# Kernel optimization log

Measured on AMD Instinct MI355X. Metric: run time of the kernel, lower is better.

## Reference

```python
import jax, jax.numpy as jnp
import numpy as np

N = 100000
E = 1600000
HID = 128
EPS = 1e-8


def _linear_params(key, fan_in, fan_out, bias=True, gain=1.0):
    kw, kb = jax.random.split(key)
    bound = gain / np.sqrt(fan_in)
    W = jax.random.uniform(kw, (fan_in, fan_out), jnp.float32, -bound, bound)
    if bias:
        b = jax.random.uniform(kb, (fan_out,), jnp.float32, -bound, bound)
        return W, b
    return W


def setup_inputs() -> dict:
    key = jax.random.key(0)
    ks = jax.random.split(key, 12)
    h = jax.random.normal(ks[0], (N, HID), jnp.float32)
    coord = jax.random.normal(ks[1], (N, 3), jnp.float32)
    edge_index = jax.random.randint(ks[2], (2, E), 0, N, jnp.int64)
    # edge_mlp: Linear(2*HID+1 -> HID), SiLU, Linear(HID -> HID), SiLU
    We1, be1 = _linear_params(ks[3], 2 * HID + 1, HID)
    We2, be2 = _linear_params(ks[4], HID, HID)
    # node_mlp: Linear(2*HID -> HID), SiLU, Linear(HID -> HID)
    Wn1, bn1 = _linear_params(ks[5], 2 * HID, HID)
    Wn2, bn2 = _linear_params(ks[6], HID, HID)
    # coord_mlp: Linear(HID -> HID), SiLU, Linear(HID -> 1, no bias, xavier gain=0.001)
    Wc1, bc1 = _linear_params(ks[7], HID, HID)
    Wc2 = _linear_params(ks[8], HID, 1, bias=False, gain=0.001 * np.sqrt(6.0 * HID / (HID + 1)))
    return {
        "h": h, "edge_index": edge_index, "coord": coord,
        "We1": We1, "be1": be1, "We2": We2, "be2": be2,
        "Wn1": Wn1, "bn1": bn1, "Wn2": Wn2, "bn2": bn2,
        "Wc1": Wc1, "bc1": bc1, "Wc2": Wc2,
    }


def _egcl(h, edge_index, coord, We1, be1, We2, be2, Wn1, bn1, Wn2, bn2, Wc1, bc1, Wc2):
    row, col = edge_index[0], edge_index[1]
    n = h.shape[0]
    # coord2radial (normalize=True, detach on norm)
    coord_diff = coord[row] - coord[col]                       # [E,3]
    radial = jnp.sum(coord_diff ** 2, axis=1, keepdims=True)   # [E,1]
    norm = jax.lax.stop_gradient(jnp.sqrt(radial)) + EPS
    coord_diff = coord_diff / norm
    # edge_model (no edge_attr, no attention)
    edge_in = jnp.concatenate([h[row], h[col], radial], axis=1)  # [E, 2H+1]
    m = jax.nn.silu(edge_in @ We1 + be1)
    m = jax.nn.silu(m @ We2 + be2)                               # [E,H]
    # coord_model (coords_agg='mean', tanh=False)
    phi_x = jax.nn.silu(m @ Wc1 + bc1) @ Wc2                     # [E,1]
    trans = coord_diff * phi_x                                   # [E,3]
    agg_c = jax.ops.segment_sum(trans, row, num_segments=n)
    cnt = jax.ops.segment_sum(jnp.ones((trans.shape[0],), trans.dtype), row, num_segments=n)
    agg_c = agg_c / jnp.clip(cnt, 1.0, None)[:, None]
    coord_out = coord + agg_c
    # node_model (residual=True)
    agg_h = jax.ops.segment_sum(m, row, num_segments=n)          # [N,H]
    node_in = jnp.concatenate([h, agg_h], axis=1)
    out = jax.nn.silu(node_in @ Wn1 + bn1) @ Wn2 + bn2
    h_out = h + out
    return h_out, coord_out


def reference(h, edge_index, coord, We1, be1, We2, be2, Wn1, bn1, Wn2, bn2, Wc1, bc1, Wc2):
    return _egcl(h, edge_index, coord, We1, be1, We2, be2, Wn1, bn1, Wn2, bn2, Wc1, bc1, Wc2)
```

## Files before the change

### kernel.cpp

```cpp
#include <hip/hip_runtime.h>

#define NN 100000
#define NE 1600000
#define HD 128
#define EPSV 1e-8f
#define EB 64
#define LPAD 136
#define CPAD 264

typedef unsigned short ushort_t;
typedef __attribute__((ext_vector_type(8))) short bf16x8;
typedef __attribute__((ext_vector_type(4))) float f32x4;

__device__ __forceinline__ float silu_f(float x) {
    return x * __builtin_amdgcn_rcpf(1.0f + __expf(-x));
}
__device__ __forceinline__ float b2f(unsigned short u) {
    union { unsigned int i; float f; } v; v.i = ((unsigned int)u) << 16; return v.f;
}
__device__ __forceinline__ unsigned short f2b(float f) {
    union { float f; unsigned int i; } v; v.f = f;
    unsigned int r = v.i + 0x7fff + ((v.i >> 16) & 1);
    return (unsigned short)(r >> 16);
}
__device__ __forceinline__ unsigned int cvt_pk_bf16(float lo, float hi) {
    unsigned int r;
    asm("v_cvt_pk_bf16_f32 %0, %1, %2" : "=v"(r) : "v"(lo), "v"(hi));
    return r;
}

extern "C" __global__ __launch_bounds__(256)
void k_prep(const float* __restrict__ We2, const float* __restrict__ Wc1,
            const float* __restrict__ We1, const float* __restrict__ Wn1,
            const float* __restrict__ Wn2,
            ushort_t* __restrict__ We2T, ushort_t* __restrict__ Wc1T,
            ushort_t* __restrict__ WabT, ushort_t* __restrict__ Wn1T,
            ushort_t* __restrict__ Wn2T)
{
    int id = blockIdx.x * 256 + threadIdx.x;
    if (id < 16384) {
        int n = id >> 7, k = id & 127;
        We2T[id] = f2b(We2[k * HD + n]);
    } else if (id < 32768) {
        int r = id - 16384; int n = r >> 7, k = r & 127;
        Wc1T[r] = f2b(Wc1[k * HD + n]);
    } else if (id < 65536) {
        int r = id - 32768; int j = r >> 7, k = r & 127;
        float v = (j < 128) ? We1[k * HD + j] : We1[(size_t)(128 + k) * HD + (j - 128)];
        WabT[r] = f2b(v);
    } else if (id < 98304) {
        int r = id - 65536; int j = r >> 8, k = r & 255;
        Wn1T[r] = f2b(Wn1[(size_t)k * HD + j]);
    } else if (id < 114688) {
        int r = id - 98304; int j = r >> 7, k = r & 127;
        Wn2T[r] = f2b(Wn2[k * HD + j]);
    }
}

extern "C" __global__ __launch_bounds__(256)
void k_hist(const int* __restrict__ ei, int* __restrict__ deg)
{
    int e = blockIdx.x * 256 + threadIdx.x;
    atomicAdd(&deg[ei[e]], 1);
}

extern "C" __global__ __launch_bounds__(1024)
void k_scan1(const int* __restrict__ deg, int* __restrict__ bsum)
{
    __shared__ int wsum[16];
    const int tid = threadIdx.x;
    const int lane = tid & 63, w = tid >> 6;
    int i = blockIdx.x * 1024 + tid;
    int v = (i < NN) ? deg[i] : 0;
#pragma unroll
    for (int off = 32; off > 0; off >>= 1) v += __shfl_xor(v, off, 64);
    if (lane == 0) wsum[w] = v;
    __syncthreads();
    if (tid == 0) {
        int s = 0;
#pragma unroll
        for (int k = 0; k < 16; k++) s += wsum[k];
        bsum[blockIdx.x] = s;
    }
}

extern "C" __global__ __launch_bounds__(128)
void k_scan2(const int* __restrict__ bsum, int* __restrict__ boff, int nb)
{
    __shared__ int wsum2[2];
    const int tid = threadIdx.x;
    const int lane = tid & 63, w = tid >> 6;
    int v = (tid < nb) ? bsum[tid] : 0;
    int s = v;
#pragma unroll
    for (int off = 1; off < 64; off <<= 1) {
        int t = __shfl_up(s, off, 64);
        if (lane >= off) s += t;
    }
    if (lane == 63) wsum2[w] = s;
    __syncthreads();
    int excl = ((w == 1) ? wsum2[0] : 0) + s - v;
    if (tid < nb) boff[tid] = excl;
}

extern "C" __global__ __launch_bounds__(1024)
void k_scan3(const int* __restrict__ deg, const int* __restrict__ boff,
             int* __restrict__ cursor)
{
    __shared__ int wsum[16];
    const int tid = threadIdx.x;
    const int lane = tid & 63, w = tid >> 6;
    int i = blockIdx.x * 1024 + tid;
    int v = (i < NN) ? deg[i] : 0;
    int s = v;
#pragma unroll
    for (int off = 1; off < 64; off <<= 1) {
        int t = __shfl_up(s, off, 64);
        if (lane >= off) s += t;
    }
    if (lane == 63) wsum[w] = s;
    __syncthreads();
    if (w == 0) {
        int ws = (lane < 16) ? wsum[lane] : 0;
#pragma unroll
        for (int off = 1; off < 16; off <<= 1) {
            int t = __shfl_up(ws, off, 64);
            if (lane >= off) ws += t;
        }
        if (lane < 16) wsum[lane] = ws;
    }
    __syncthreads();
    int excl = boff[blockIdx.x] + ((w > 0) ? wsum[w - 1] : 0) + s - v;
    if (i < NN) cursor[i] = excl;
}

extern "C" __global__ __launch_bounds__(256)
void k_sortids(const int* __restrict__ ei, int* __restrict__ cursor,
               int2* __restrict__ rc)
{
    int e = blockIdx.x * 256 + threadIdx.x;
    int r = ei[e], c = ei[NE + e];
    int slot = atomicAdd(&cursor[r], 1);
    rc[slot] = make_int2(r, c);
}

extern "C" __global__ __launch_bounds__(256)
void k_ab(const float* __restrict__ h, const ushort_t* __restrict__ WabT,
          const float* __restrict__ be1,
          ushort_t* __restrict__ A, ushort_t* __restrict__ B)
{
    __shared__ ushort_t hs[64][LPAD] __attribute__((aligned(16)));
    const int tid = threadIdx.x;
    const int n0 = blockIdx.x * 64;
    {
        int r = tid >> 2, seg = tid & 3;
        int n = n0 + r; if (n >= NN) n = n0;
        const float4* src = (const float4*)(h + (size_t)n * HD + seg * 32);
        uint2* dst = (uint2*)&hs[r][seg * 32];
#pragma unroll
        for (int i = 0; i < 8; i++) {
            float4 v = src[i];
            uint2 p; p.x = cvt_pk_bf16(v.x, v.y); p.y = cvt_pk_bf16(v.z, v.w);
            dst[i] = p;
        }
    }
    __syncthreads();
    const int wave = tid >> 6, lane = tid & 63;
    const int lr = lane & 15, lg = lane >> 4;
    f32x4 acc[16];
#pragma unroll
    for (int nt = 0; nt < 16; nt++) acc[nt] = (f32x4){0.f, 0.f, 0.f, 0.f};
#pragma unroll
    for (int ks = 0; ks < 4; ks++) {
        bf16x8 hf8 = *(const bf16x8*)&hs[wave * 16 + lr][ks * 32 + lg * 8];
#pragma unroll
        for (int nt = 0; nt < 16; nt++) {
            bf16x8 wf = *(const bf16x8*)(WabT + (size_t)(nt * 16 + lr) * HD + ks * 32 + lg * 8);
            acc[nt] = __builtin_amdgcn_mfma_f32_16x16x32_bf16(wf, hf8, acc[nt], 0, 0, 0);
        }
    }
    const int node = n0 + wave * 16 + lr;
    if (node < NN) {
#pragma unroll
        for (int nt = 0; nt < 16; nt++) {
            float4 bias = (nt < 8) ? ((const float4*)be1)[nt * 4 + lg]
                                   : (float4){0.f, 0.f, 0.f, 0.f};
            uint2 pk;
            pk.x = cvt_pk_bf16(acc[nt][0] + bias.x, acc[nt][1] + bias.y);
            pk.y = cvt_pk_bf16(acc[nt][2] + bias.z, acc[nt][3] + bias.w);
            if (nt < 8)
                *(uint2*)(A + (size_t)node * HD + nt * 16 + lg * 4) = pk;
            else
                *(uint2*)(B + (size_t)node * HD + (nt - 8) * 16 + lg * 4) = pk;
        }
    }
}

extern "C" __global__ __launch_bounds__(128, 4)
void k_edge(const int2* __restrict__ rc, const float* __restrict__ coord,
            const ushort_t* __restrict__ A, const ushort_t* __restrict__ B,
            const float* __restrict__ WeL, const float* __restrict__ be2,
            const ushort_t* __restrict__ We2T,
            const ushort_t* __restrict__ Wc1T,
            const float* __restrict__ bc1, const float* __restrict__ Wc2,
            float* __restrict__ agg_h, float* __restrict__ agg_c)
{
    __shared__ ushort_t m_lds[EB][LPAD] __attribute__((aligned(16)));
    __shared__ float cd_lds[EB][3];
    __shared__ int rows_s[EB];
    __shared__ float bias_lds[384] __attribute__((aligned(16)));
    __shared__ float wel_lds[128] __attribute__((aligned(16)));

    const int tid = threadIdx.x;
    const int e  = tid >> 1;
    const int hf = tid & 1;
    const int wave = tid >> 6, lane = tid & 63;
    const int lr = lane & 15, lg = lane >> 4;

    {
        int i = tid;
        bias_lds[i]       = (i < 128) ? be2[i] : 0.f;
        bias_lds[128 + i] = bc1[i];
        if (i < 128) bias_lds[256 + i] = Wc2[i];
        wel_lds[i] = WeL[i];
    }
    int2 rce = rc[blockIdx.x * EB + e];
    const int row = rce.x, col = rce.y;

    float c0 = coord[(size_t)row * 3 + 0] - coord[(size_t)col * 3 + 0];
    float c1 = coord[(size_t)row * 3 + 1] - coord[(size_t)col * 3 + 1];
    float c2 = coord[(size_t)row * 3 + 2] - coord[(size_t)col * 3 + 2];
    float radial = c0 * c0 + c1 * c1 + c2 * c2;
    if (hf == 0) {
        rows_s[e] = row;
        float inv = __builtin_amdgcn_rcpf(sqrtf(radial) + EPSV);
        cd_lds[e][0] = c0 * inv; cd_lds[e][1] = c1 * inv; cd_lds[e][2] = c2 * inv;
    }
    __syncthreads();

    {
        const bf16x8* A8 = (const bf16x8*)(A + (size_t)row * HD + hf * 64);
        const bf16x8* B8 = (const bf16x8*)(B + (size_t)col * HD + hf * 64);
        const float4* WL4 = (const float4*)wel_lds + hf * 16;
#pragma unroll
        for (int i = 0; i < 8; i++) {
            bf16x8 av = A8[i], bv = B8[i];
            float4 w0 = WL4[2 * i], w1 = WL4[2 * i + 1];
            float v0 = silu_f(b2f((ushort_t)av[0]) + b2f((ushort_t)bv[0]) + radial * w0.x);
            float v1 = silu_f(b2f((ushort_t)av[1]) + b2f((ushort_t)bv[1]) + radial * w0.y);
            float v2 = silu_f(b2f((ushort_t)av[2]) + b2f((ushort_t)bv[2]) + radial * w0.z);
            float v3 = silu_f(b2f((ushort_t)av[3]) + b2f((ushort_t)bv[3]) + radial * w0.w);
            float v4 = silu_f(b2f((ushort_t)av[4]) + b2f((ushort_t)bv[4]) + radial * w1.x);
            float v5 = silu_f(b2f((ushort_t)av[5]) + b2f((ushort_t)bv[5]) + radial * w1.y);
            float v6 = silu_f(b2f((ushort_t)av[6]) + b2f((ushort_t)bv[6]) + radial * w1.z);
            float v7 = silu_f(b2f((ushort_t)av[7]) + b2f((ushort_t)bv[7]) + radial * w1.w);
            uint4 p;
            p.x = cvt_pk_bf16(v0, v1); p.y = cvt_pk_bf16(v2, v3);
            p.z = cvt_pk_bf16(v4, v5); p.w = cvt_pk_bf16(v6, v7);
            *(uint4*)&m_lds[e][hf * 64 + i * 8] = p;
        }
    }

    f32x4 acc[2][8];
#pragma unroll
    for (int mt = 0; mt < 2; mt++)
#pragma unroll
        for (int nt = 0; nt < 8; nt++) acc[mt][nt] = (f32x4){0.f, 0.f, 0.f, 0.f};
#pragma unroll
    for (int ks = 0; ks < 4; ks++) {
        bf16x8 mf0 = *(const bf16x8*)&m_lds[wave * 32 + lr][ks * 32 + lg * 8];
        bf16x8 mf1 = *(const bf16x8*)&m_lds[wave * 32 + 16 + lr][ks * 32 + lg * 8];
#pragma unroll
        for (int nt = 0; nt < 8; nt++) {
            bf16x8 wf = *(const bf16x8*)(We2T + (size_t)(nt * 16 + lr) * HD + ks * 32 + lg * 8);
            acc[0][nt] = __builtin_amdgcn_mfma_f32_16x16x32_bf16(wf, mf0, acc[0][nt], 0, 0, 0);
            acc[1][nt] = __builtin_amdgcn_mfma_f32_16x16x32_bf16(wf, mf1, acc[1][nt], 0, 0, 0);
        }
    }
#pragma unroll
    for (int nt = 0; nt < 8; nt++) {
        float4 be2v = *(const float4*)&bias_lds[nt * 16 + lg * 4];
#pragma unroll
        for (int mt = 0; mt < 2; mt++) {
            float v0 = silu_f(acc[mt][nt][0] + be2v.x);
            float v1 = silu_f(acc[mt][nt][1] + be2v.y);
            float v2 = silu_f(acc[mt][nt][2] + be2v.z);
            float v3 = silu_f(acc[mt][nt][3] + be2v.w);
            uint2 pk; pk.x = cvt_pk_bf16(v0, v1); pk.y = cvt_pk_bf16(v2, v3);
            *(uint2*)&m_lds[wave * 32 + mt * 16 + lr][nt * 16 + lg * 4] = pk;
        }
    }

#pragma unroll
    for (int mt = 0; mt < 2; mt++)
#pragma unroll
        for (int nt = 0; nt < 8; nt++) acc[mt][nt] = (f32x4){0.f, 0.f, 0.f, 0.f};
#pragma unroll
    for (int ks = 0; ks < 4; ks++) {
        bf16x8 mf0 = *(const bf16x8*)&m_lds[wave * 32 + lr][ks * 32 + lg * 8];
        bf16x8 mf1 = *(const bf16x8*)&m_lds[wave * 32 + 16 + lr][ks * 32 + lg * 8];
#pragma unroll
        for (int nt = 0; nt < 8; nt++) {
            bf16x8 wf = *(const bf16x8*)(Wc1T + (size_t)(nt * 16 + lr) * HD + ks * 32 + lg * 8);
            acc[0][nt] = __builtin_amdgcn_mfma_f32_16x16x32_bf16(wf, mf0, acc[0][nt], 0, 0, 0);
            acc[1][nt] = __builtin_amdgcn_mfma_f32_16x16x32_bf16(wf, mf1, acc[1][nt], 0, 0, 0);
        }
    }

    float ph0 = 0.f, ph1 = 0.f;
#pragma unroll
    for (int nt = 0; nt < 8; nt++) {
        float4 bc1v = *(const float4*)&bias_lds[128 + nt * 16 + lg * 4];
        float4 wc2v = *(const float4*)&bias_lds[256 + nt * 16 + lg * 4];
        ph0 += silu_f(acc[0][nt][0] + bc1v.x) * wc2v.x
             + silu_f(acc[0][nt][1] + bc1v.y) * wc2v.y
             + silu_f(acc[0][nt][2] + bc1v.z) * wc2v.z
             + silu_f(acc[0][nt][3] + bc1v.w) * wc2v.w;
        ph1 += silu_f(acc[1][nt][0] + bc1v.x) * wc2v.x
             + silu_f(acc[1][nt][1] + bc1v.y) * wc2v.y
             + silu_f(acc[1][nt][2] + bc1v.z) * wc2v.z
             + silu_f(acc[1][nt][3] + bc1v.w) * wc2v.w;
    }
    ph0 += __shfl_xor(ph0, 16, 64); ph0 += __shfl_xor(ph0, 32, 64);
    ph1 += __shfl_xor(ph1, 16, 64); ph1 += __shfl_xor(ph1, 32, 64);
    if (lg == 0) {
        int e0 = wave * 32 + lr, e1 = e0 + 16;
        cd_lds[e0][0] *= ph0; cd_lds[e0][1] *= ph0; cd_lds[e0][2] *= ph0;
        cd_lds[e1][0] *= ph1; cd_lds[e1][1] *= ph1; cd_lds[e1][2] *= ph1;
    }

    __syncthreads();

    {
        const int j = tid;
        float acc_r = 0.f;
        int cur = rows_s[0];
        for (int es = 0; es < EB; es++) {
            int r = rows_s[es];
            if (r != cur) {
                atomicAdd(&agg_h[(size_t)cur * HD + j], acc_r);
                acc_r = 0.f; cur = r;
            }
            acc_r += b2f(m_lds[es][j]);
        }
        atomicAdd(&agg_h[(size_t)cur * HD + j], acc_r);
    }
    if (wave == 0) {
        int c = lane >> 4, sub = lane & 15;
        if (c < 3) {
            const int es0 = sub * 4, es1 = es0 + 4;
            float acc_r = 0.f;
            int cur = rows_s[es0];
            for (int es = es0; es < es1; es++) {
                int r = rows_s[es];
                if (r != cur) {
                    atomicAdd(&agg_c[(size_t)cur * 3 + c], acc_r);
                    acc_r = 0.f; cur = r;
                }
                acc_r += cd_lds[es][c];
            }
            atomicAdd(&agg_c[(size_t)cur * 3 + c], acc_r);
        }
    }
}

extern "C" __global__ __launch_bounds__(256)
void k_node(const float* __restrict__ h, const ushort_t* __restrict__ Wn1T,
            const float* __restrict__ bn1, const ushort_t* __restrict__ Wn2T,
            const float* __restrict__ bn2, const float* __restrict__ coord,
            const int* __restrict__ deg,
            float* __restrict__ hout ,
            float* __restrict__ cout )
{
    __shared__ ushort_t cs[64][CPAD] __attribute__((aligned(16)));
    __shared__ ushort_t us[64][LPAD] __attribute__((aligned(16)));
    const int tid = threadIdx.x;
    const int n0 = blockIdx.x * 64;
    {
        int r = tid >> 2, seg = tid & 3;
        int n = n0 + r; if (n >= NN) n = n0;
        const float4* s0 = (const float4*)(h + (size_t)n * HD + seg * 32);
        const float4* s1 = (const float4*)(hout + (size_t)n * HD + seg * 32);
        uint2* d0 = (uint2*)&cs[r][seg * 32];
        uint2* d1 = (uint2*)&cs[r][128 + seg * 32];
#pragma unroll
        for (int i = 0; i < 8; i++) {
            float4 v = s0[i];
            uint2 p; p.x = cvt_pk_bf16(v.x, v.y); p.y = cvt_pk_bf16(v.z, v.w);
            d0[i] = p;
            float4 w = s1[i];
            uint2 q; q.x = cvt_pk_bf16(w.x, w.y); q.y = cvt_pk_bf16(w.z, w.w);
            d1[i] = q;
        }
    }
    __syncthreads();
    const int wave = tid >> 6, lane = tid & 63;
    const int lr = lane & 15, lg = lane >> 4;

    f32x4 acc[8];
#pragma unroll
    for (int nt = 0; nt < 8; nt++) acc[nt] = (f32x4){0.f, 0.f, 0.f, 0.f};
#pragma unroll
    for (int ks = 0; ks < 8; ks++) {
        bf16x8 cf = *(const bf16x8*)&cs[wave * 16 + lr][ks * 32 + lg * 8];
#pragma unroll
        for (int nt = 0; nt < 8; nt++) {
            bf16x8 wf = *(const bf16x8*)(Wn1T + (size_t)(nt * 16 + lr) * 256 + ks * 32 + lg * 8);
            acc[nt] = __builtin_amdgcn_mfma_f32_16x16x32_bf16(wf, cf, acc[nt], 0, 0, 0);
        }
    }
#pragma unroll
    for (int nt = 0; nt < 8; nt++) {
        float4 b1 = ((const float4*)bn1)[nt * 4 + lg];
        float v0 = silu_f(acc[nt][0] + b1.x);
        float v1 = silu_f(acc[nt][1] + b1.y);
        float v2 = silu_f(acc[nt][2] + b1.z);
        float v3 = silu_f(acc[nt][3] + b1.w);
        uint2 pk; pk.x = cvt_pk_bf16(v0, v1); pk.y = cvt_pk_bf16(v2, v3);
        *(uint2*)&us[wave * 16 + lr][nt * 16 + lg * 4] = pk;
    }

    f32x4 acc2[8];
#pragma unroll
    for (int nt = 0; nt < 8; nt++) acc2[nt] = (f32x4){0.f, 0.f, 0.f, 0.f};
#pragma unroll
    for (int ks = 0; ks < 4; ks++) {
        bf16x8 uf = *(const bf16x8*)&us[wave * 16 + lr][ks * 32 + lg * 8];
#pragma unroll
        for (int nt = 0; nt < 8; nt++) {
            bf16x8 wf = *(const bf16x8*)(Wn2T + (size_t)(nt * 16 + lr) * HD + ks * 32 + lg * 8);
            acc2[nt] = __builtin_amdgcn_mfma_f32_16x16x32_bf16(wf, uf, acc2[nt], 0, 0, 0);
        }
    }
    const int node = n0 + wave * 16 + lr;
    if (node < NN) {
#pragma unroll
        for (int nt = 0; nt < 8; nt++) {
            float4 b2 = ((const float4*)bn2)[nt * 4 + lg];
            size_t idx = (size_t)node * HD + nt * 16 + lg * 4;
            float4 hv = *(const float4*)(h + idx);
            float4 o;
            o.x = hv.x + acc2[nt][0] + b2.x;
            o.y = hv.y + acc2[nt][1] + b2.y;
            o.z = hv.z + acc2[nt][2] + b2.z;
            o.w = hv.w + acc2[nt][3] + b2.w;
            *(float4*)(hout + idx) = o;
        }
        if (lg == 0) {
            float invc = __builtin_amdgcn_rcpf(fmaxf((float)deg[node], 1.0f));
#pragma unroll
            for (int i = 0; i < 3; i++) {
                size_t idx = (size_t)node * 3 + i;
                cout[idx] = coord[idx] + cout[idx] * invc;
            }
        }
    }
}

extern "C" void kernel_launch(void* const* d_in, const int* in_sizes, int n_in,
                              void* d_out, int out_size, void* d_ws, size_t ws_size,
                              hipStream_t stream)
{
    const float* h     = (const float*)d_in[0];
    const int*   ei    = (const int*)d_in[1];
    const float* coord = (const float*)d_in[2];
    const float* We1   = (const float*)d_in[3];
    const float* be1   = (const float*)d_in[4];
    const float* We2   = (const float*)d_in[5];
    const float* be2   = (const float*)d_in[6];
    const float* Wn1   = (const float*)d_in[7];
    const float* bn1   = (const float*)d_in[8];
    const float* Wn2   = (const float*)d_in[9];
    const float* bn2   = (const float*)d_in[10];
    const float* Wc1   = (const float*)d_in[11];
    const float* bc1   = (const float*)d_in[12];
    const float* Wc2   = (const float*)d_in[13];

    float* out   = (float*)d_out;
    float* agg_h = out;
    float* agg_c = out + (size_t)NN * HD;

    ushort_t* A    = (ushort_t*)d_ws;
    ushort_t* B    = A + (size_t)NN * HD;
    ushort_t* We2T = B + (size_t)NN * HD;
    ushort_t* Wc1T = We2T + 16384;
    ushort_t* WabT = Wc1T + 16384;
    ushort_t* Wn1T = WabT + 32768;
    ushort_t* Wn2T = Wn1T + 32768;
    int* deg    = (int*)(Wn2T + 16384);
    int* cursor = deg + NN;
    int* bsum   = cursor + NN;
    int* boff   = bsum + 128;
    int2* rc    = (int2*)(boff + 128);
    const float* WeL = We1 + (size_t)2 * HD * HD;

    const int scan_nb = (NN + 1023) / 1024;

    hipMemsetAsync(d_out, 0, (size_t)out_size * sizeof(float), stream);
    hipMemsetAsync(deg, 0, (size_t)NN * sizeof(int), stream);

    k_prep<<<448, 256, 0, stream>>>(We2, Wc1, We1, Wn1, Wn2,
                                    We2T, Wc1T, WabT, Wn1T, Wn2T);
    k_hist<<<NE / 256, 256, 0, stream>>>(ei, deg);
    k_ab<<<(NN + 63) / 64, 256, 0, stream>>>(h, WabT, be1, A, B);
    k_scan1<<<scan_nb, 1024, 0, stream>>>(deg, bsum);
    k_scan2<<<1, 128, 0, stream>>>(bsum, boff, scan_nb);
    k_scan3<<<scan_nb, 1024, 0, stream>>>(deg, boff, cursor);
    k_sortids<<<NE / 256, 256, 0, stream>>>(ei, cursor, rc);
    k_edge<<<NE / EB, 128, 0, stream>>>(rc, coord, A, B, WeL, be2,
                                        We2T, Wc1T, bc1, Wc2, agg_h, agg_c);
    k_node<<<(NN + 63) / 64, 256, 0, stream>>>(h, Wn1T, bn1, Wn2T, bn2, coord,
                                               deg, agg_h, agg_c);
}
```

Before: 889.1 us.

## Fuse prep with histogram, drop scan2 launch, load MFMA fragments directly

Merges the weight-prep and degree-histogram kernels into one launch, and folds the block-offset scan into k_scan3 by having each block sum the preceding block sums itself. k_ab and k_node now build MFMA fragments directly from global fp32 memory instead of staging through LDS with a barrier. s_setprio is added around the MFMA loops in k_edge. The aim is fewer launches and less LDS traffic, at the cost of uncoalesced fragment loads from global memory and redundant bsum reads in the scan.

After: 897.9 us. No clear change (+1.0%).

```diff
diff --git a/kernel.cpp b/kernel.cpp
--- a/kernel.cpp
+++ b/kernel.cpp
@@ -6,7 +6,6 @@
 #define EPSV 1e-8f
 #define EB 64
 #define LPAD 136
-#define CPAD 264
 
 typedef unsigned short ushort_t;
 typedef __attribute__((ext_vector_type(8))) short bf16x8;
@@ -28,16 +27,26 @@
     asm("v_cvt_pk_bf16_f32 %0, %1, %2" : "=v"(r) : "v"(lo), "v"(hi));
     return r;
 }
+__device__ __forceinline__ bf16x8 frag_from_f32(const float* p) {
+    float4 a0 = *(const float4*)p;
+    float4 a1 = *(const float4*)(p + 4);
+    union { bf16x8 v; uint4 u; } r;
+    r.u.x = cvt_pk_bf16(a0.x, a0.y); r.u.y = cvt_pk_bf16(a0.z, a0.w);
+    r.u.z = cvt_pk_bf16(a1.x, a1.y); r.u.w = cvt_pk_bf16(a1.z, a1.w);
+    return r.v;
+}
 
 extern "C" __global__ __launch_bounds__(256)
-void k_prep(const float* __restrict__ We2, const float* __restrict__ Wc1,
-            const float* __restrict__ We1, const float* __restrict__ Wn1,
-            const float* __restrict__ Wn2,
-            ushort_t* __restrict__ We2T, ushort_t* __restrict__ Wc1T,
-            ushort_t* __restrict__ WabT, ushort_t* __restrict__ Wn1T,
-            ushort_t* __restrict__ Wn2T)
+void k_prep_hist(const int* __restrict__ ei, int* __restrict__ deg,
+                 const float* __restrict__ We2, const float* __restrict__ Wc1,
+                 const float* __restrict__ We1, const float* __restrict__ Wn1,
+                 const float* __restrict__ Wn2,
+                 ushort_t* __restrict__ We2T, ushort_t* __restrict__ Wc1T,
+                 ushort_t* __restrict__ WabT, ushort_t* __restrict__ Wn1T,
+                 ushort_t* __restrict__ Wn2T)
 {
     int id = blockIdx.x * 256 + threadIdx.x;
+    atomicAdd(&deg[ei[id]], 1);
     if (id < 16384) {
         int n = id >> 7, k = id & 127;
         We2T[id] = f2b(We2[k * HD + n]);
@@ -57,13 +66,6 @@
     }
 }
 
-extern "C" __global__ __launch_bounds__(256)
-void k_hist(const int* __restrict__ ei, int* __restrict__ deg)
-{
-    int e = blockIdx.x * 256 + threadIdx.x;
-    atomicAdd(&deg[ei[e]], 1);
-}
-
 extern "C" __global__ __launch_bounds__(1024)
 void k_scan1(const int* __restrict__ deg, int* __restrict__ bsum)
 {
@@ -84,30 +86,12 @@
     }
 }
 
-extern "C" __global__ __launch_bounds__(128)
-void k_scan2(const int* __restrict__ bsum, int* __restrict__ boff, int nb)
-{
-    __shared__ int wsum2[2];
-    const int tid = threadIdx.x;
-    const int lane = tid & 63, w = tid >> 6;
-    int v = (tid < nb) ? bsum[tid] : 0;
-    int s = v;
-#pragma unroll
-    for (int off = 1; off < 64; off <<= 1) {
-        int t = __shfl_up(s, off, 64);
-        if (lane >= off) s += t;
-    }
-    if (lane == 63) wsum2[w] = s;
-    __syncthreads();
-    int excl = ((w == 1) ? wsum2[0] : 0) + s - v;
-    if (tid < nb) boff[tid] = excl;
-}
-
 extern "C" __global__ __launch_bounds__(1024)
-void k_scan3(const int* __restrict__ deg, const int* __restrict__ boff,
+void k_scan3(const int* __restrict__ deg, const int* __restrict__ bsum,
              int* __restrict__ cursor)
 {
     __shared__ int wsum[16];
+    __shared__ int boff_s;
     const int tid = threadIdx.x;
     const int lane = tid & 63, w = tid >> 6;
     int i = blockIdx.x * 1024 + tid;
@@ -119,6 +103,13 @@
         if (lane >= off) s += t;
     }
     if (lane == 63) wsum[w] = s;
+    if (w == 0) {
+        int a = 0;
+        for (int k = lane; k < blockIdx.x; k += 64) a += bsum[k];
+#pragma unroll
+        for (int off = 32; off > 0; off >>= 1) a += __shfl_xor(a, off, 64);
+        if (lane == 0) boff_s = a;
+    }
     __syncthreads();
     if (w == 0) {
         int ws = (lane < 16) ? wsum[lane] : 0;
@@ -130,7 +121,7 @@
         if (lane < 16) wsum[lane] = ws;
     }
     __syncthreads();
-    int excl = boff[blockIdx.x] + ((w > 0) ? wsum[w - 1] : 0) + s - v;
+    int excl = boff_s + ((w > 0) ? wsum[w - 1] : 0) + s - v;
     if (i < NN) cursor[i] = excl;
 }
 
@@ -149,37 +140,25 @@
           const float* __restrict__ be1,
           ushort_t* __restrict__ A, ushort_t* __restrict__ B)
 {
-    __shared__ ushort_t hs[64][LPAD] __attribute__((aligned(16)));
     const int tid = threadIdx.x;
     const int n0 = blockIdx.x * 64;
-    {
-        int r = tid >> 2, seg = tid & 3;
-        int n = n0 + r; if (n >= NN) n = n0;
-        const float4* src = (const float4*)(h + (size_t)n * HD + seg * 32);
-        uint2* dst = (uint2*)&hs[r][seg * 32];
-#pragma unroll
-        for (int i = 0; i < 8; i++) {
-            float4 v = src[i];
-            uint2 p; p.x = cvt_pk_bf16(v.x, v.y); p.y = cvt_pk_bf16(v.z, v.w);
-            dst[i] = p;
-        }
-    }
-    __syncthreads();
     const int wave = tid >> 6, lane = tid & 63;
     const int lr = lane & 15, lg = lane >> 4;
+    const int node = n0 + wave * 16 + lr;
+    const int nsrc = (node < NN) ? node : (NN - 1);
+
     f32x4 acc[16];
 #pragma unroll
     for (int nt = 0; nt < 16; nt++) acc[nt] = (f32x4){0.f, 0.f, 0.f, 0.f};
 #pragma unroll
     for (int ks = 0; ks < 4; ks++) {
-        bf16x8 hf8 = *(const bf16x8*)&hs[wave * 16 + lr][ks * 32 + lg * 8];
+        bf16x8 hf8 = frag_from_f32(h + (size_t)nsrc * HD + ks * 32 + lg * 8);
 #pragma unroll
         for (int nt = 0; nt < 16; nt++) {
             bf16x8 wf = *(const bf16x8*)(WabT + (size_t)(nt * 16 + lr) * HD + ks * 32 + lg * 8);
             acc[nt] = __builtin_amdgcn_mfma_f32_16x16x32_bf16(wf, hf8, acc[nt], 0, 0, 0);
         }
     }
-    const int node = n0 + wave * 16 + lr;
     if (node < NN) {
 #pragma unroll
         for (int nt = 0; nt < 16; nt++) {
@@ -219,9 +198,9 @@
 
     {
         int i = tid;
-        bias_lds[i]       = (i < 128) ? be2[i] : 0.f;
+        bias_lds[i]       = be2[i];
         bias_lds[128 + i] = bc1[i];
-        if (i < 128) bias_lds[256 + i] = Wc2[i];
+        bias_lds[256 + i] = Wc2[i];
         wel_lds[i] = WeL[i];
     }
     int2 rce = rc[blockIdx.x * EB + e];
@@ -266,6 +245,7 @@
     for (int mt = 0; mt < 2; mt++)
 #pragma unroll
         for (int nt = 0; nt < 8; nt++) acc[mt][nt] = (f32x4){0.f, 0.f, 0.f, 0.f};
+    __builtin_amdgcn_s_setprio(1);
 #pragma unroll
     for (int ks = 0; ks < 4; ks++) {
         bf16x8 mf0 = *(const bf16x8*)&m_lds[wave * 32 + lr][ks * 32 + lg * 8];
@@ -277,6 +257,7 @@
             acc[1][nt] = __builtin_amdgcn_mfma_f32_16x16x32_bf16(wf, mf1, acc[1][nt], 0, 0, 0);
         }
     }
+    __builtin_amdgcn_s_setprio(0);
 #pragma unroll
     for (int nt = 0; nt < 8; nt++) {
         float4 be2v = *(const float4*)&bias_lds[nt * 16 + lg * 4];
@@ -295,6 +276,7 @@
     for (int mt = 0; mt < 2; mt++)
 #pragma unroll
         for (int nt = 0; nt < 8; nt++) acc[mt][nt] = (f32x4){0.f, 0.f, 0.f, 0.f};
+    __builtin_amdgcn_s_setprio(1);
 #pragma unroll
     for (int ks = 0; ks < 4; ks++) {
         bf16x8 mf0 = *(const bf16x8*)&m_lds[wave * 32 + lr][ks * 32 + lg * 8];
@@ -306,6 +288,7 @@
             acc[1][nt] = __builtin_amdgcn_mfma_f32_16x16x32_bf16(wf, mf1, acc[1][nt], 0, 0, 0);
         }
     }
+    __builtin_amdgcn_s_setprio(0);
 
     float ph0 = 0.f, ph1 = 0.f;
 #pragma unroll
@@ -372,37 +355,22 @@
             float* __restrict__ hout ,
             float* __restrict__ cout )
 {
-    __shared__ ushort_t cs[64][CPAD] __attribute__((aligned(16)));
     __shared__ ushort_t us[64][LPAD] __attribute__((aligned(16)));
     const int tid = threadIdx.x;
     const int n0 = blockIdx.x * 64;
-    {
-        int r = tid >> 2, seg = tid & 3;
-        int n = n0 + r; if (n >= NN) n = n0;
-        const float4* s0 = (const float4*)(h + (size_t)n * HD + seg * 32);
-        const float4* s1 = (const float4*)(hout + (size_t)n * HD + seg * 32);
-        uint2* d0 = (uint2*)&cs[r][seg * 32];
-        uint2* d1 = (uint2*)&cs[r][128 + seg * 32];
-#pragma unroll
-        for (int i = 0; i < 8; i++) {
-            float4 v = s0[i];
-            uint2 p; p.x = cvt_pk_bf16(v.x, v.y); p.y = cvt_pk_bf16(v.z, v.w);
-            d0[i] = p;
-            float4 w = s1[i];
-            uint2 q; q.x = cvt_pk_bf16(w.x, w.y); q.y = cvt_pk_bf16(w.z, w.w);
-            d1[i] = q;
-        }
-    }
-    __syncthreads();
     const int wave = tid >> 6, lane = tid & 63;
     const int lr = lane & 15, lg = lane >> 4;
+    const int node = n0 + wave * 16 + lr;
+    const int nsrc = (node < NN) ? node : (NN - 1);
 
     f32x4 acc[8];
 #pragma unroll
     for (int nt = 0; nt < 8; nt++) acc[nt] = (f32x4){0.f, 0.f, 0.f, 0.f};
 #pragma unroll
     for (int ks = 0; ks < 8; ks++) {
-        bf16x8 cf = *(const bf16x8*)&cs[wave * 16 + lr][ks * 32 + lg * 8];
+        const float* src = (ks < 4) ? (h + (size_t)nsrc * HD + ks * 32 + lg * 8)
+                                    : (hout + (size_t)nsrc * HD + (ks - 4) * 32 + lg * 8);
+        bf16x8 cf = frag_from_f32(src);
 #pragma unroll
         for (int nt = 0; nt < 8; nt++) {
             bf16x8 wf = *(const bf16x8*)(Wn1T + (size_t)(nt * 16 + lr) * 256 + ks * 32 + lg * 8);
@@ -432,7 +400,6 @@
             acc2[nt] = __builtin_amdgcn_mfma_f32_16x16x32_bf16(wf, uf, acc2[nt], 0, 0, 0);
         }
     }
-    const int node = n0 + wave * 16 + lr;
     if (node < NN) {
 #pragma unroll
         for (int nt = 0; nt < 8; nt++) {
@@ -490,8 +457,7 @@
     int* deg    = (int*)(Wn2T + 16384);
     int* cursor = deg + NN;
     int* bsum   = cursor + NN;
-    int* boff   = bsum + 128;
-    int2* rc    = (int2*)(boff + 128);
+    int2* rc    = (int2*)(bsum + 128);
     const float* WeL = We1 + (size_t)2 * HD * HD;
 
     const int scan_nb = (NN + 1023) / 1024;
@@ -499,13 +465,11 @@
     hipMemsetAsync(d_out, 0, (size_t)out_size * sizeof(float), stream);
     hipMemsetAsync(deg, 0, (size_t)NN * sizeof(int), stream);
 
-    k_prep<<<448, 256, 0, stream>>>(We2, Wc1, We1, Wn1, Wn2,
-                                    We2T, Wc1T, WabT, Wn1T, Wn2T);
-    k_hist<<<NE / 256, 256, 0, stream>>>(ei, deg);
+    k_prep_hist<<<NE / 256, 256, 0, stream>>>(ei, deg, We2, Wc1, We1, Wn1, Wn2,
+                                              We2T, Wc1T, WabT, Wn1T, Wn2T);
     k_ab<<<(NN + 63) / 64, 256, 0, stream>>>(h, WabT, be1, A, B);
     k_scan1<<<scan_nb, 1024, 0, stream>>>(deg, bsum);
-    k_scan2<<<1, 128, 0, stream>>>(bsum, boff, scan_nb);
-    k_scan3<<<scan_nb, 1024, 0, stream>>>(deg, boff, cursor);
+    k_scan3<<<scan_nb, 1024, 0, stream>>>(deg, bsum, cursor);
     k_sortids<<<NE / 256, 256, 0, stream>>>(ei, cursor, rc);
     k_edge<<<NE / EB, 128, 0, stream>>>(rc, coord, A, B, WeL, be2,
                                         We2T, Wc1T, bc1, Wc2, agg_h, agg_c);
```
